# Kernel optimization log

Measured on AMD Instinct MI355X. Metric: run time of the kernel, lower is better.

Reference implementation:

```python
import jax, jax.numpy as jnp
import numpy as np

IN_FEATURES = 256
HIDDEN_SIZE = 512
OUT_FEATURES = 256


def setup_inputs() -> dict:
    key = jax.random.key(0)
    k_x, k_w1, k_b1, k_w2, k_b2 = jax.random.split(key, 5)
    batch, seq_len = 64, 2048
    # PyTorch nn.Linear init scale ~ 1/sqrt(fan_in)
    s1 = 1.0 / np.sqrt(IN_FEATURES + HIDDEN_SIZE)
    s2 = 1.0 / np.sqrt(HIDDEN_SIZE)
    return {
        "x": jax.random.normal(k_x, (batch, seq_len, IN_FEATURES), dtype=jnp.float32),
        # W1: [hidden+in, hidden]; concat order in original is (hidden, input)
        "W1": jax.random.uniform(k_w1, (HIDDEN_SIZE + IN_FEATURES, HIDDEN_SIZE), minval=-s1, maxval=s1, dtype=jnp.float32),
        "b1": jax.random.uniform(k_b1, (HIDDEN_SIZE,), minval=-s1, maxval=s1, dtype=jnp.float32),
        "W2": jax.random.uniform(k_w2, (HIDDEN_SIZE, OUT_FEATURES), minval=-s2, maxval=s2, dtype=jnp.float32),
        "b2": jax.random.uniform(k_b2, (OUT_FEATURES,), minval=-s2, maxval=s2, dtype=jnp.float32),
    }


def reference(x, W1, b1, W2, b2):
    # x: [batch, seq, in] -> scan over seq
    batch = x.shape[0]
    # Split W1 into the hidden-part and input-part (concat order: hidden first)
    W1_h = W1[:HIDDEN_SIZE]   # [hidden, hidden]
    W1_x = W1[HIDDEN_SIZE:]   # [in, hidden]
    h0 = jnp.zeros((batch, HIDDEN_SIZE), dtype=x.dtype)

    def step(h, x_t):
        # equivalent to concat([h, x_t], -1) @ W1 + b1
        h_new = jnp.tanh(h @ W1_h + x_t @ W1_x + b1)
        y_t = h_new @ W2 + b2
        return h_new, y_t

    xs = jnp.swapaxes(x, 0, 1)              # [seq, batch, in]
    h_last, ys = jax.lax.scan(step, h0, xs)  # ys: [seq, batch, out]
    output = jnp.swapaxes(ys, 0, 1)          # [batch, seq, out]
    # original returns curr_hidden_state with leading dim 1
    return output, h_last[None, :, :]
```

## Files before the change

kernel.cpp:

```cpp
#include <hip/hip_runtime.h>
#include <math.h>


#define BB 64
#define TT 2048
#define II 256
#define HH 512
#define OO 256
#define NBLK 256
#define OUT_OFF ((size_t)BB * TT * OO)
#define FLAGS_INTS ((TT + 1) * NBLK)
#define LDV 776

typedef unsigned long long ull;
#define F4C(v,i) ((i)==0?(v).x:((i)==1?(v).y:((i)==2?(v).z:(v).w)))

__global__ void rnn_init(int* __restrict__ flags) {
    int i = blockIdx.x * blockDim.x + threadIdx.x;
    if (i < FLAGS_INTS) flags[i] = 0;
}

__global__ __launch_bounds__(256, 1) void rnn_persist(
    const float* __restrict__ x, const float* __restrict__ W1,
    const float* __restrict__ b1, const float* __restrict__ W2,
    const float* __restrict__ b2, float* __restrict__ out,
    int* __restrict__ flags, float* __restrict__ hbuf)
{
    __shared__ float v_s[16 * LDV];
    __shared__ float sc_s[16 * 8 * 32];

    const int tid = threadIdx.x;
    const int blk = blockIdx.x;
    const int bi  = blk >> 6;
    const int cj  = blk & 63;
    const int R0  = bi << 4;
    const int C0  = cj << 3;
    const int O0  = cj << 2;

    const int g  = tid & 31;
    const int r2 = tid >> 5;
    const int orow = tid >> 3, oc = tid & 7;
    const int yrow = tid >> 2, yo = tid & 3;

    float w1r[6][4][8];
    #pragma unroll
    for (int j = 0; j < 6; ++j)
        #pragma unroll
        for (int i = 0; i < 4; ++i) {
            const float* wp = W1 + (size_t)(j * 128 + (g << 2) + i) * HH + C0;
            float4 a = *(const float4*)wp;
            float4 b = *(const float4*)(wp + 4);
            w1r[j][i][0] = a.x; w1r[j][i][1] = a.y; w1r[j][i][2] = a.z; w1r[j][i][3] = a.w;
            w1r[j][i][4] = b.x; w1r[j][i][5] = b.y; w1r[j][i][6] = b.z; w1r[j][i][7] = b.w;
        }
    float w2r[4][4][4];
    #pragma unroll
    for (int j = 0; j < 4; ++j)
        #pragma unroll
        for (int i = 0; i < 4; ++i) {
            float4 a = *(const float4*)(W2 + (size_t)(j * 128 + (g << 2) + i) * OO + O0);
            w2r[j][i][0] = a.x; w2r[j][i][1] = a.y; w2r[j][i][2] = a.z; w2r[j][i][3] = a.w;
        }
    const float b1v = (tid < 128) ? b1[C0 + oc] : 0.f;
    const float b2v = (tid < 64)  ? b2[O0 + yo] : 0.f;

    const ull* hb64[2] = { (const ull*)hbuf, (const ull*)(hbuf + (size_t)BB * HH) };

    #pragma unroll
    for (int m = 0; m < 16; ++m) {
        int idx = (m << 8) + tid;
        *(ull*)&v_s[(idx >> 8) * LDV + ((idx & 255) << 1)] = 0ull;
    }
    #pragma unroll
    for (int m = 0; m < 4; ++m) {
        int idx = (m << 8) + tid;
        int row = idx >> 6, k4 = idx & 63;
        float4 xv = *(const float4*)&x[((size_t)(R0 + row) * TT + 0) * II + (k4 << 2)];
        *(float4*)&v_s[row * LDV + 512 + (k4 << 2)] = xv;
    }
    __syncthreads();

    for (int t = 0; t < TT; ++t) {
        if (t > 0) {
            if (tid < 64) {
                const int* f = flags + (size_t)t * NBLK + (bi << 6) + tid;
                while (__hip_atomic_load(f, __ATOMIC_RELAXED,
                                         __HIP_MEMORY_SCOPE_AGENT) == 0) {}
            }
            __syncthreads();
            const ull* hsrc = hb64[t & 1];
            #pragma unroll
            for (int half = 0; half < 2; ++half) {
                ull tmp[8];
                #pragma unroll
                for (int m = 0; m < 8; ++m) {
                    int idx = (((half << 3) + m) << 8) + tid;
                    tmp[m] = __hip_atomic_load(
                        (ull*)&hsrc[(size_t)(R0 + (idx >> 8)) * (HH / 2) + (idx & 255)],
                        __ATOMIC_RELAXED, __HIP_MEMORY_SCOPE_AGENT);
                }
                #pragma unroll
                for (int m = 0; m < 8; ++m) {
                    int idx = (((half << 3) + m) << 8) + tid;
                    *(ull*)&v_s[(idx >> 8) * LDV + ((idx & 255) << 1)] = tmp[m];
                }
            }
            __syncthreads();
        }

        float pa[2][8];
        #pragma unroll
        for (int rr = 0; rr < 2; ++rr)
            #pragma unroll
            for (int c = 0; c < 8; ++c) pa[rr][c] = 0.f;
        #pragma unroll
        for (int rr = 0; rr < 2; ++rr) {
            const int row = r2 + (rr << 3);
            #pragma unroll
            for (int j = 0; j < 6; ++j) {
                float4 vv = *(const float4*)&v_s[row * LDV + j * 128 + (g << 2)];
                #pragma unroll
                for (int i = 0; i < 4; ++i) {
                    const float vi = F4C(vv, i);
                    #pragma unroll
                    for (int c = 0; c < 8; ++c)
                        pa[rr][c] = fmaf(vi, w1r[j][i][c], pa[rr][c]);
                }
            }
        }
        #pragma unroll
        for (int rr = 0; rr < 2; ++rr)
            #pragma unroll
            for (int c = 0; c < 8; ++c)
                sc_s[(((r2 + (rr << 3)) << 3) + c) * 32 + (g ^ (c << 2))] = pa[rr][c];
        __syncthreads();
        if (tid < 128) {
            float s = 0.f;
            #pragma unroll
            for (int j = 0; j < 8; ++j) {
                float4 q = *(const float4*)&sc_s[(tid << 5) + ((j << 2) ^ (oc << 2))];
                s += (q.x + q.y) + (q.z + q.w);
            }
            float hnew = tanhf(s + b1v);
            float* hdst = hbuf + (size_t)((t + 1) & 1) * (BB * HH);
            __hip_atomic_store(&hdst[(size_t)(R0 + orow) * HH + C0 + oc], hnew,
                               __ATOMIC_RELAXED, __HIP_MEMORY_SCOPE_AGENT);
            if (t == TT - 1)
                out[OUT_OFF + (size_t)(R0 + orow) * HH + C0 + oc] = hnew;
        }
        asm volatile("s_waitcnt vmcnt(0)" ::: "memory");
        __syncthreads();
        if (tid == 0)
            __hip_atomic_store((int*)&flags[(size_t)(t + 1) * NBLK + blk], 1,
                               __ATOMIC_RELAXED, __HIP_MEMORY_SCOPE_AGENT);

        if (t + 1 < TT) {
            #pragma unroll
            for (int m = 0; m < 4; ++m) {
                int idx = (m << 8) + tid;
                int row = idx >> 6, k4 = idx & 63;
                float4 xv = *(const float4*)&x[((size_t)(R0 + row) * TT + (t + 1)) * II + (k4 << 2)];
                *(float4*)&v_s[row * LDV + 512 + (k4 << 2)] = xv;
            }
        }

        if (t > 0) {
            float py[2][4];
            #pragma unroll
            for (int rr = 0; rr < 2; ++rr)
                #pragma unroll
                for (int o = 0; o < 4; ++o) py[rr][o] = 0.f;
            #pragma unroll
            for (int rr = 0; rr < 2; ++rr) {
                const int row = r2 + (rr << 3);
                #pragma unroll
                for (int j = 0; j < 4; ++j) {
                    float4 vv = *(const float4*)&v_s[row * LDV + j * 128 + (g << 2)];
                    #pragma unroll
                    for (int i = 0; i < 4; ++i) {
                        const float vi = F4C(vv, i);
                        #pragma unroll
                        for (int o = 0; o < 4; ++o)
                            py[rr][o] = fmaf(vi, w2r[j][i][o], py[rr][o]);
                    }
                }
            }
            #pragma unroll
            for (int rr = 0; rr < 2; ++rr)
                #pragma unroll
                for (int o = 0; o < 4; ++o)
                    sc_s[(((r2 + (rr << 3)) << 2) + o) * 32 + (g ^ (o << 2))] = py[rr][o];
            __syncthreads();
            if (tid < 64) {
                float s = 0.f;
                #pragma unroll
                for (int j = 0; j < 8; ++j) {
                    float4 q = *(const float4*)&sc_s[(tid << 5) + ((j << 2) ^ (yo << 2))];
                    s += (q.x + q.y) + (q.z + q.w);
                }
                out[((size_t)(R0 + yrow) * TT + (t - 1)) * OO + O0 + yo] = s + b2v;
            }
        }
    }

    if (tid < 64) {
        const int* f = flags + (size_t)TT * NBLK + (bi << 6) + tid;
        while (__hip_atomic_load(f, __ATOMIC_RELAXED,
                                 __HIP_MEMORY_SCOPE_AGENT) == 0) {}
    }
    __syncthreads();
    {
        const ull* hsrc = hb64[TT & 1];
        #pragma unroll
        for (int half = 0; half < 2; ++half) {
            ull tmp[8];
            #pragma unroll
            for (int m = 0; m < 8; ++m) {
                int idx = (((half << 3) + m) << 8) + tid;
                tmp[m] = __hip_atomic_load(
                    (ull*)&hsrc[(size_t)(R0 + (idx >> 8)) * (HH / 2) + (idx & 255)],
                    __ATOMIC_RELAXED, __HIP_MEMORY_SCOPE_AGENT);
            }
            #pragma unroll
            for (int m = 0; m < 8; ++m) {
                int idx = (((half << 3) + m) << 8) + tid;
                *(ull*)&v_s[(idx >> 8) * LDV + ((idx & 255) << 1)] = tmp[m];
            }
        }
        __syncthreads();
        float py[2][4];
        #pragma unroll
        for (int rr = 0; rr < 2; ++rr)
            #pragma unroll
            for (int o = 0; o < 4; ++o) py[rr][o] = 0.f;
        #pragma unroll
        for (int rr = 0; rr < 2; ++rr) {
            const int row = r2 + (rr << 3);
            #pragma unroll
            for (int j = 0; j < 4; ++j) {
                float4 vv = *(const float4*)&v_s[row * LDV + j * 128 + (g << 2)];
                #pragma unroll
                for (int i = 0; i < 4; ++i) {
                    const float vi = F4C(vv, i);
                    #pragma unroll
                    for (int o = 0; o < 4; ++o)
                        py[rr][o] = fmaf(vi, w2r[j][i][o], py[rr][o]);
                }
            }
        }
        #pragma unroll
        for (int rr = 0; rr < 2; ++rr)
            #pragma unroll
            for (int o = 0; o < 4; ++o)
                sc_s[(((r2 + (rr << 3)) << 2) + o) * 32 + (g ^ (o << 2))] = py[rr][o];
        __syncthreads();
        if (tid < 64) {
            float s = 0.f;
            #pragma unroll
            for (int j = 0; j < 8; ++j) {
                float4 q = *(const float4*)&sc_s[(tid << 5) + ((j << 2) ^ (yo << 2))];
                s += (q.x + q.y) + (q.z + q.w);
            }
            out[((size_t)(R0 + yrow) * TT + (TT - 1)) * OO + O0 + yo] = s + b2v;
        }
    }
}

extern "C" void kernel_launch(void* const* d_in, const int* in_sizes, int n_in,
                              void* d_out, int out_size, void* d_ws, size_t ws_size,
                              hipStream_t stream) {
    const float* x  = (const float*)d_in[0];
    const float* W1 = (const float*)d_in[1];
    const float* b1 = (const float*)d_in[2];
    const float* W2 = (const float*)d_in[3];
    const float* b2 = (const float*)d_in[4];
    float* out = (float*)d_out;

    int*   flags = (int*)d_ws;
    float* hbuf  = (float*)((char*)d_ws + (size_t)FLAGS_INTS * sizeof(int));

    rnn_init<<<dim3((FLAGS_INTS + 255) / 256), dim3(256), 0, stream>>>(flags);
    rnn_persist<<<dim3(NBLK), dim3(256), 0, stream>>>(x, W1, b1, W2, b2, out,
                                                      flags, hbuf);
}
```

Baseline: 11.06 ms.

## Load h directly into registers, use monotonic tags, overlap output projection reduction

Removes the shared-memory staging of the hidden state and x. Each thread now loads its own h slice from global memory with atomic 64-bit loads, and its x slice straight into registers. The per-step flag array is replaced by monotonic per-block counters, split into two halves so each 64-thread group signals independently, and 128 threads poll instead of 64. The W2 output projection is computed in the same pass as the W1 product, and its reduction runs concurrently on threads 128-191, which cuts the number of block barriers per step. The trade-off is more polling traffic and redundant global reads of h across threads.

```diff
diff --git a/kernel.cpp b/kernel.cpp
--- a/kernel.cpp
+++ b/kernel.cpp
@@ -9,25 +9,32 @@
 #define OO 256
 #define NBLK 256
 #define OUT_OFF ((size_t)BB * TT * OO)
-#define FLAGS_INTS ((TT + 1) * NBLK)
-#define LDV 776
+#define NTAGS (4 * 64 * 2)
 
 typedef unsigned long long ull;
 #define F4C(v,i) ((i)==0?(v).x:((i)==1?(v).y:((i)==2?(v).z:(v).w)))
 
-__global__ void rnn_init(int* __restrict__ flags) {
+__global__ void rnn_init(int* __restrict__ tags) {
     int i = blockIdx.x * blockDim.x + threadIdx.x;
-    if (i < FLAGS_INTS) flags[i] = 0;
+    if (i < NTAGS) tags[i] = 0;
+}
+
+__device__ inline float4 ld_h4(const ull* p) {
+    ull a = __hip_atomic_load(p,     __ATOMIC_RELAXED, __HIP_MEMORY_SCOPE_AGENT);
+    ull b = __hip_atomic_load(p + 1, __ATOMIC_RELAXED, __HIP_MEMORY_SCOPE_AGENT);
+    float2 lo = __builtin_bit_cast(float2, a);
+    float2 hi = __builtin_bit_cast(float2, b);
+    return make_float4(lo.x, lo.y, hi.x, hi.y);
 }
 
 __global__ __launch_bounds__(256, 1) void rnn_persist(
     const float* __restrict__ x, const float* __restrict__ W1,
     const float* __restrict__ b1, const float* __restrict__ W2,
     const float* __restrict__ b2, float* __restrict__ out,
-    int* __restrict__ flags, float* __restrict__ hbuf)
+    int* __restrict__ tags, float* __restrict__ hbuf)
 {
-    __shared__ float v_s[16 * LDV];
-    __shared__ float sc_s[16 * 8 * 32];
+    __shared__ float sc_h[16 * 8 * 32];
+    __shared__ float sc_y[16 * 4 * 32];
 
     const int tid = threadIdx.x;
     const int blk = blockIdx.x;
@@ -39,8 +46,8 @@
 
     const int g  = tid & 31;
     const int r2 = tid >> 5;
-    const int orow = tid >> 3, oc = tid & 7;
-    const int yrow = tid >> 2, yo = tid & 3;
+    const int oc = tid & 7;
+    const int yi = tid - 128, yo = yi & 3, yrow = yi >> 2;
 
     float w1r[6][4][8];
     #pragma unroll
@@ -62,63 +69,57 @@
             w2r[j][i][0] = a.x; w2r[j][i][1] = a.y; w2r[j][i][2] = a.z; w2r[j][i][3] = a.w;
         }
     const float b1v = (tid < 128) ? b1[C0 + oc] : 0.f;
-    const float b2v = (tid < 64)  ? b2[O0 + yo] : 0.f;
-
-    const ull* hb64[2] = { (const ull*)hbuf, (const ull*)(hbuf + (size_t)BB * HH) };
-
-    #pragma unroll
-    for (int m = 0; m < 16; ++m) {
-        int idx = (m << 8) + tid;
-        *(ull*)&v_s[(idx >> 8) * LDV + ((idx & 255) << 1)] = 0ull;
-    }
-    #pragma unroll
-    for (int m = 0; m < 4; ++m) {
-        int idx = (m << 8) + tid;
-        int row = idx >> 6, k4 = idx & 63;
-        float4 xv = *(const float4*)&x[((size_t)(R0 + row) * TT + 0) * II + (k4 << 2)];
-        *(float4*)&v_s[row * LDV + 512 + (k4 << 2)] = xv;
-    }
-    __syncthreads();
+    const float b2v = (tid >= 128 && tid < 192) ? b2[O0 + yo] : 0.f;
+
+    ull* hb[2] = { (ull*)hbuf, (ull*)(hbuf + (size_t)BB * HH) };
+    int* mytag = &tags[((bi << 6) + cj) * 2];
+    const int* ptag = &tags[((bi << 6) + (tid >> 1)) * 2 + (tid & 1)];
 
     for (int t = 0; t < TT; ++t) {
+        float4 xreg[2][2];
+        #pragma unroll
+        for (int rr = 0; rr < 2; ++rr)
+            #pragma unroll
+            for (int jx = 0; jx < 2; ++jx)
+                xreg[rr][jx] = *(const float4*)&x[((size_t)(R0 + r2 + (rr << 3)) * TT + t) * II
+                                                  + jx * 128 + (g << 2)];
+        float4 hreg[2][4];
         if (t > 0) {
-            if (tid < 64) {
-                const int* f = flags + (size_t)t * NBLK + (bi << 6) + tid;
-                while (__hip_atomic_load(f, __ATOMIC_RELAXED,
-                                         __HIP_MEMORY_SCOPE_AGENT) == 0) {}
-            }
+            if (tid < 128)
+                while (__hip_atomic_load(ptag, __ATOMIC_RELAXED,
+                                         __HIP_MEMORY_SCOPE_AGENT) < t) {}
             __syncthreads();
-            const ull* hsrc = hb64[t & 1];
-            #pragma unroll
-            for (int half = 0; half < 2; ++half) {
-                ull tmp[8];
-                #pragma unroll
-                for (int m = 0; m < 8; ++m) {
-                    int idx = (((half << 3) + m) << 8) + tid;
-                    tmp[m] = __hip_atomic_load(
-                        (ull*)&hsrc[(size_t)(R0 + (idx >> 8)) * (HH / 2) + (idx & 255)],
-                        __ATOMIC_RELAXED, __HIP_MEMORY_SCOPE_AGENT);
-                }
-                #pragma unroll
-                for (int m = 0; m < 8; ++m) {
-                    int idx = (((half << 3) + m) << 8) + tid;
-                    *(ull*)&v_s[(idx >> 8) * LDV + ((idx & 255) << 1)] = tmp[m];
-                }
-            }
+            const ull* hsrc = hb[t & 1];
+            #pragma unroll
+            for (int rr = 0; rr < 2; ++rr) {
+                const ull* rp = hsrc + (size_t)(R0 + r2 + (rr << 3)) * (HH / 2) + (g << 1);
+                #pragma unroll
+                for (int j = 0; j < 4; ++j)
+                    hreg[rr][j] = ld_h4(rp + j * 64);
+            }
+        } else {
+            #pragma unroll
+            for (int rr = 0; rr < 2; ++rr)
+                #pragma unroll
+                for (int j = 0; j < 4; ++j)
+                    hreg[rr][j] = make_float4(0.f, 0.f, 0.f, 0.f);
             __syncthreads();
         }
 
         float pa[2][8];
-        #pragma unroll
-        for (int rr = 0; rr < 2; ++rr)
+        float py[2][4];
+        #pragma unroll
+        for (int rr = 0; rr < 2; ++rr) {
             #pragma unroll
             for (int c = 0; c < 8; ++c) pa[rr][c] = 0.f;
-        #pragma unroll
-        for (int rr = 0; rr < 2; ++rr) {
-            const int row = r2 + (rr << 3);
+            #pragma unroll
+            for (int o = 0; o < 4; ++o) py[rr][o] = 0.f;
+        }
+        #pragma unroll
+        for (int rr = 0; rr < 2; ++rr) {
             #pragma unroll
             for (int j = 0; j < 6; ++j) {
-                float4 vv = *(const float4*)&v_s[row * LDV + j * 128 + (g << 2)];
+                float4 vv = (j < 4) ? hreg[rr][j] : xreg[rr][j - 4];
                 #pragma unroll
                 for (int i = 0; i < 4; ++i) {
                     const float vi = F4C(vv, i);
@@ -127,55 +128,10 @@
                         pa[rr][c] = fmaf(vi, w1r[j][i][c], pa[rr][c]);
                 }
             }
-        }
-        #pragma unroll
-        for (int rr = 0; rr < 2; ++rr)
-            #pragma unroll
-            for (int c = 0; c < 8; ++c)
-                sc_s[(((r2 + (rr << 3)) << 3) + c) * 32 + (g ^ (c << 2))] = pa[rr][c];
-        __syncthreads();
-        if (tid < 128) {
-            float s = 0.f;
-            #pragma unroll
-            for (int j = 0; j < 8; ++j) {
-                float4 q = *(const float4*)&sc_s[(tid << 5) + ((j << 2) ^ (oc << 2))];
-                s += (q.x + q.y) + (q.z + q.w);
-            }
-            float hnew = tanhf(s + b1v);
-            float* hdst = hbuf + (size_t)((t + 1) & 1) * (BB * HH);
-            __hip_atomic_store(&hdst[(size_t)(R0 + orow) * HH + C0 + oc], hnew,
-                               __ATOMIC_RELAXED, __HIP_MEMORY_SCOPE_AGENT);
-            if (t == TT - 1)
-                out[OUT_OFF + (size_t)(R0 + orow) * HH + C0 + oc] = hnew;
-        }
-        asm volatile("s_waitcnt vmcnt(0)" ::: "memory");
-        __syncthreads();
-        if (tid == 0)
-            __hip_atomic_store((int*)&flags[(size_t)(t + 1) * NBLK + blk], 1,
-                               __ATOMIC_RELAXED, __HIP_MEMORY_SCOPE_AGENT);
-
-        if (t + 1 < TT) {
-            #pragma unroll
-            for (int m = 0; m < 4; ++m) {
-                int idx = (m << 8) + tid;
-                int row = idx >> 6, k4 = idx & 63;
-                float4 xv = *(const float4*)&x[((size_t)(R0 + row) * TT + (t + 1)) * II + (k4 << 2)];
-                *(float4*)&v_s[row * LDV + 512 + (k4 << 2)] = xv;
-            }
-        }
-
-        if (t > 0) {
-            float py[2][4];
-            #pragma unroll
-            for (int rr = 0; rr < 2; ++rr)
-                #pragma unroll
-                for (int o = 0; o < 4; ++o) py[rr][o] = 0.f;
-            #pragma unroll
-            for (int rr = 0; rr < 2; ++rr) {
-                const int row = r2 + (rr << 3);
+            if (t > 0) {
                 #pragma unroll
                 for (int j = 0; j < 4; ++j) {
-                    float4 vv = *(const float4*)&v_s[row * LDV + j * 128 + (g << 2)];
+                    float4 vv = hreg[rr][j];
                     #pragma unroll
                     for (int i = 0; i < 4; ++i) {
                         const float vi = F4C(vv, i);
@@ -185,60 +141,70 @@
                     }
                 }
             }
-            #pragma unroll
-            for (int rr = 0; rr < 2; ++rr)
+        }
+        #pragma unroll
+        for (int rr = 0; rr < 2; ++rr) {
+            const int row = r2 + (rr << 3);
+            #pragma unroll
+            for (int c = 0; c < 8; ++c)
+                sc_h[((row << 3) + c) * 32 + (g ^ (c << 2))] = pa[rr][c];
+            if (t > 0)
                 #pragma unroll
                 for (int o = 0; o < 4; ++o)
-                    sc_s[(((r2 + (rr << 3)) << 2) + o) * 32 + (g ^ (o << 2))] = py[rr][o];
-            __syncthreads();
-            if (tid < 64) {
-                float s = 0.f;
-                #pragma unroll
-                for (int j = 0; j < 8; ++j) {
-                    float4 q = *(const float4*)&sc_s[(tid << 5) + ((j << 2) ^ (yo << 2))];
-                    s += (q.x + q.y) + (q.z + q.w);
-                }
-                out[((size_t)(R0 + yrow) * TT + (t - 1)) * OO + O0 + yo] = s + b2v;
-            }
+                    sc_y[((row << 2) + o) * 32 + (g ^ (o << 2))] = py[rr][o];
+        }
+        __syncthreads();
+
+        if (tid < 128) {
+            float s = 0.f;
+            #pragma unroll
+            for (int j = 0; j < 8; ++j) {
+                float4 q = *(const float4*)&sc_h[(tid << 5) + ((j << 2) ^ (oc << 2))];
+                s += (q.x + q.y) + (q.z + q.w);
+            }
+            float hnew = tanhf(s + b1v);
+            float* hdst = (float*)hb[(t + 1) & 1];
+            __hip_atomic_store(&hdst[(size_t)(R0 + (tid >> 3)) * HH + C0 + oc], hnew,
+                               __ATOMIC_RELAXED, __HIP_MEMORY_SCOPE_AGENT);
+            if (t == TT - 1)
+                out[OUT_OFF + (size_t)(R0 + (tid >> 3)) * HH + C0 + oc] = hnew;
+            asm volatile("s_waitcnt vmcnt(0)" ::: "memory");
+            if ((tid & 63) == 0)
+                __hip_atomic_store(&mytag[tid >> 6], t + 1,
+                                   __ATOMIC_RELAXED, __HIP_MEMORY_SCOPE_AGENT);
+        } else if (tid < 192 && t > 0) {
+            float s = 0.f;
+            #pragma unroll
+            for (int j = 0; j < 8; ++j) {
+                float4 q = *(const float4*)&sc_y[(yi << 5) + ((j << 2) ^ (yo << 2))];
+                s += (q.x + q.y) + (q.z + q.w);
+            }
+            out[((size_t)(R0 + yrow) * TT + (t - 1)) * OO + O0 + yo] = s + b2v;
         }
     }
 
-    if (tid < 64) {
-        const int* f = flags + (size_t)TT * NBLK + (bi << 6) + tid;
-        while (__hip_atomic_load(f, __ATOMIC_RELAXED,
-                                 __HIP_MEMORY_SCOPE_AGENT) == 0) {}
-    }
+    if (tid < 128)
+        while (__hip_atomic_load(ptag, __ATOMIC_RELAXED,
+                                 __HIP_MEMORY_SCOPE_AGENT) < TT) {}
     __syncthreads();
     {
-        const ull* hsrc = hb64[TT & 1];
-        #pragma unroll
-        for (int half = 0; half < 2; ++half) {
-            ull tmp[8];
-            #pragma unroll
-            for (int m = 0; m < 8; ++m) {
-                int idx = (((half << 3) + m) << 8) + tid;
-                tmp[m] = __hip_atomic_load(
-                    (ull*)&hsrc[(size_t)(R0 + (idx >> 8)) * (HH / 2) + (idx & 255)],
-                    __ATOMIC_RELAXED, __HIP_MEMORY_SCOPE_AGENT);
-            }
-            #pragma unroll
-            for (int m = 0; m < 8; ++m) {
-                int idx = (((half << 3) + m) << 8) + tid;
-                *(ull*)&v_s[(idx >> 8) * LDV + ((idx & 255) << 1)] = tmp[m];
-            }
-        }
-        __syncthreads();
+        float4 hreg[2][4];
+        const ull* hsrc = hb[TT & 1];
+        #pragma unroll
+        for (int rr = 0; rr < 2; ++rr) {
+            const ull* rp = hsrc + (size_t)(R0 + r2 + (rr << 3)) * (HH / 2) + (g << 1);
+            #pragma unroll
+            for (int j = 0; j < 4; ++j)
+                hreg[rr][j] = ld_h4(rp + j * 64);
+        }
         float py[2][4];
         #pragma unroll
-        for (int rr = 0; rr < 2; ++rr)
+        for (int rr = 0; rr < 2; ++rr) {
             #pragma unroll
             for (int o = 0; o < 4; ++o) py[rr][o] = 0.f;
-        #pragma unroll
-        for (int rr = 0; rr < 2; ++rr) {
-            const int row = r2 + (rr << 3);
             #pragma unroll
             for (int j = 0; j < 4; ++j) {
-                float4 vv = *(const float4*)&v_s[row * LDV + j * 128 + (g << 2)];
+                float4 vv = hreg[rr][j];
                 #pragma unroll
                 for (int i = 0; i < 4; ++i) {
                     const float vi = F4C(vv, i);
@@ -247,18 +213,17 @@
                         py[rr][o] = fmaf(vi, w2r[j][i][o], py[rr][o]);
                 }
             }
-        }
-        #pragma unroll
-        for (int rr = 0; rr < 2; ++rr)
+            const int row = r2 + (rr << 3);
             #pragma unroll
             for (int o = 0; o < 4; ++o)
-                sc_s[(((r2 + (rr << 3)) << 2) + o) * 32 + (g ^ (o << 2))] = py[rr][o];
+                sc_y[((row << 2) + o) * 32 + (g ^ (o << 2))] = py[rr][o];
+        }
         __syncthreads();
-        if (tid < 64) {
+        if (tid >= 128 && tid < 192) {
             float s = 0.f;
             #pragma unroll
             for (int j = 0; j < 8; ++j) {
-                float4 q = *(const float4*)&sc_s[(tid << 5) + ((j << 2) ^ (yo << 2))];
+                float4 q = *(const float4*)&sc_y[(yi << 5) + ((j << 2) ^ (yo << 2))];
                 s += (q.x + q.y) + (q.z + q.w);
             }
             out[((size_t)(R0 + yrow) * TT + (TT - 1)) * OO + O0 + yo] = s + b2v;
@@ -276,10 +241,10 @@
     const float* b2 = (const float*)d_in[4];
     float* out = (float*)d_out;
 
-    int*   flags = (int*)d_ws;
-    float* hbuf  = (float*)((char*)d_ws + (size_t)FLAGS_INTS * sizeof(int));
-
-    rnn_init<<<dim3((FLAGS_INTS + 255) / 256), dim3(256), 0, stream>>>(flags);
+    int*   tags = (int*)d_ws;
+    float* hbuf = (float*)((char*)d_ws + 4096);
+
+    rnn_init<<<dim3(2), dim3(256), 0, stream>>>(tags);
     rnn_persist<<<dim3(NBLK), dim3(256), 0, stream>>>(x, W1, b1, W2, b2, out,
-                                                      flags, hbuf);
-}
+                                                      tags, hbuf);
+}
```

Result: slower. 12.44 ms (+12.5%).
